# Optimization experiments

Hardware: AMD Instinct MI355X
Metric: run time of the kernel (lower is better)

## Reference

```python
import jax, jax.numpy as jnp
import numpy as np

IN_DIM = 256
HID = 384
HEADS = 6
NH1 = HID // HEADS  # 64 per-head hidden in layer1
N = 3072
SLOPE_GAT = 0.2   # LeakyReLU inside GAT attention
SLOPE_ACT = 0.01  # default nn.LeakyReLU / F.leaky_relu slope


def _leaky(x, s):
    return jnp.where(x >= 0, x, s * x)


def _gat_sublayer(h, mask, W, a, heads, nh, concat):
    # h: [N, F_in], mask: [N, N] bool, W: [heads*nh, F_in], a: [2*nh]
    n = h.shape[0]
    g = (h @ W.T).reshape(n, heads, nh)  # [N, H, F]
    # e[i,j,h] = leakyrelu(<g_i, a_l> + <g_j, a_r>)  (avoids O(N^2) concat)
    sl = jnp.einsum('nhf,f->nh', g, a[:nh])
    sr = jnp.einsum('nhf,f->nh', g, a[nh:])
    e = _leaky(sl[:, None, :] + sr[None, :, :], SLOPE_GAT)  # [N, N, H]
    e = jnp.where(mask[:, :, None], e, jnp.float32(-10000.0))
    att = jax.nn.softmax(e, axis=1)  # softmax over source nodes j
    out = jnp.einsum('ijh,jhf->ihf', att, g)
    return out.reshape(n, heads * nh) if concat else out.mean(axis=1)


def _gat(x, mask, W1, a1, W2, a2):
    x = _gat_sublayer(x, mask, W1, a1, HEADS, NH1, True)   # [N, HID]
    x = jax.nn.elu(x)
    return _gat_sublayer(x, mask, W2, a2, 1, IN_DIM, False)  # [N, IN_DIM]


def setup_inputs() -> dict:
    key = jax.random.key(0)
    ks = iter(jax.random.split(key, 32))
    d = {
        'feature': jax.random.normal(next(ks), (1, N, IN_DIM), jnp.float32),
        'adj': jax.random.randint(next(ks), (1, N, N), 0, 2, jnp.int32),
        'doc_num': 16,
        'sect_num': 192,
    }
    def w(shape, scale=0.05):
        return jax.random.normal(next(ks), shape, jnp.float32) * scale
    for br in ('sent', 'sect', 'doc'):
        d[f'W1_{br}'] = w((HID, IN_DIM))
        d[f'a1_{br}'] = w((2 * NH1,))
        d[f'W2_{br}'] = w((IN_DIM, HID))
        d[f'a2_{br}'] = w((2 * IN_DIM,))
    d['fusion_W'] = w((IN_DIM, 3 * IN_DIM)); d['fusion_b'] = jnp.zeros((IN_DIM,), jnp.float32)
    d['ffn_W0'] = w((HID, IN_DIM)); d['ffn_b0'] = jnp.zeros((HID,), jnp.float32)
    d['ffn_W1'] = w((HID, HID)); d['ffn_b1'] = jnp.zeros((HID,), jnp.float32)
    d['ffn_W2'] = w((IN_DIM, HID)); d['ffn_b2'] = jnp.zeros((IN_DIM,), jnp.float32)
    return d


def reference(feature, adj, doc_num, sect_num,
              W1_sent, a1_sent, W2_sent, a2_sent,
              W1_sect, a1_sect, W2_sect, a2_sect,
              W1_doc, a1_doc, W2_doc, a2_doc,
              fusion_W, fusion_b,
              ffn_W0, ffn_b0, ffn_W1, ffn_b1, ffn_W2, ffn_b2):
    f = feature[0]          # [N, D]
    n = f.shape[0]
    A = adj[0] != 0         # [N, N]
    cols = jnp.arange(n)
    sent_mask = A & (cols < n - sect_num - doc_num)[None, :]
    sect_mask = A & (cols >= n - sect_num - doc_num)[None, :] & (cols < n - doc_num)[None, :]
    doc_mask = A & (cols >= n - doc_num)[None, :]

    f_sent = _gat(f, sent_mask, W1_sent, a1_sent, W2_sent, a2_sent) + f
    f_sect = _gat(f, sect_mask, W1_sect, a1_sect, W2_sect, a2_sect) + f
    f_doc = _gat(f, doc_mask, W1_doc, a1_doc, W2_doc, a2_doc) + f

    fused = jnp.concatenate([f_doc, f_sect, f_sent], axis=-1)  # [N, 3D]
    fused = _leaky(fused @ fusion_W.T + fusion_b, SLOPE_ACT)
    h = _leaky(fused @ ffn_W0.T + ffn_b0, SLOPE_ACT)
    h = _leaky(h @ ffn_W1.T + ffn_b1, SLOPE_ACT)
    h = _leaky(h @ ffn_W2.T + ffn_b2, SLOPE_ACT)
    return (h + f)[None]    # [1, N, D]
```

## Files before the change

kernel.cpp:

```cpp
#include <hip/hip_runtime.h>
#include <stdint.h>

#define N_NODES 3072
#define D_IN    256
#define HIDDEN  384
#define HEADS   6
#define NH1     64
#define C1      1152
#define C2      768
#define MASK_ULL   48
#define MT_STRIDE  ((size_t)384 * N_NODES)
#define QS      6
#define LOG2E   1.4426950408889634f

typedef __bf16 bf16;
typedef __bf16 bf16x8 __attribute__((ext_vector_type(8)));
typedef __bf16 bf16x4 __attribute__((ext_vector_type(4)));
typedef float  f32x4  __attribute__((ext_vector_type(4)));

typedef __attribute__((address_space(1))) const unsigned int as1_u32;
typedef __attribute__((address_space(3))) unsigned int as3_u32;

__device__ __forceinline__ void gload_lds16(const void* g, void* l) {
  __builtin_amdgcn_global_load_lds((as1_u32*)g, (as3_u32*)l, 16, 0, 0);
}
__device__ __forceinline__ void gload_lds4(const void* g, void* l) {
  __builtin_amdgcn_global_load_lds((as1_u32*)g, (as3_u32*)l, 4, 0, 0);
}

__device__ __forceinline__ void atomAddF(float* p, float v) {
  __hip_atomic_fetch_add(p, v, __ATOMIC_RELAXED, __HIP_MEMORY_SCOPE_AGENT);
}
__device__ __forceinline__ float fexp2(float x) {
  float r; asm("v_exp_f32 %0, %1" : "=v"(r) : "v"(x)); return r;
}
__device__ __forceinline__ int bnd32(int jlo, int jhi, int len, int q, int Qb) {
  return (q >= Qb) ? ((jhi + 31) & ~31) : ((jlo + (len * q) / Qb) & ~31);
}

struct CastArgs {
  const float* src[11];
  bf16*        dst[11];
  int          cum4[12];
  int          castN;
};

__global__ __launch_bounds__(256) void prep_kernel(CastArgs A,
                                                   const int* __restrict__ adj,
                                                   unsigned char* __restrict__ maskT,
                                                   const int* __restrict__ dnum,
                                                   const int* __restrict__ snum) {
  if ((int)blockIdx.x < A.castN) {
    int g = blockIdx.x * 256 + threadIdx.x;
    int j = 0;
#pragma unroll
    for (int k = 1; k < 11; ++k) j += (g >= A.cum4[k]);
    int e = (g - A.cum4[j]) * 4;
    float4 v = *(const float4*)(A.src[j] + e);
    bf16x4 o = { (bf16)v.x, (bf16)v.y, (bf16)v.z, (bf16)v.w };
    *(bf16x4*)(A.dst[j] + e) = o;
    return;
  }
  int dn = dnum[0], sn = snum[0];
  int bb1 = N_NODES - sn - dn, bb2 = N_NODES - dn;
  int row = blockIdx.x - A.castN;
  const int* ar = adj + (size_t)row * N_NODES;
  int lane = threadIdx.x & 63, wave = threadIdx.x >> 6;
#pragma unroll
  for (int it = 0; it < N_NODES / 256; ++it) {
    int j = it * 256 + wave * 64 + lane;
    bool a = ar[j] != 0;
    unsigned long long m0 = __ballot(a && (j < bb1));
    unsigned long long m1 = __ballot(a && (j >= bb1) && (j < bb2));
    unsigned long long m2 = __ballot(a && (j >= bb2));
    int moBase = it * 32 + wave * 8;
    if (lane < 8)
      maskT[(size_t)(moBase + lane) * N_NODES + row] = (unsigned char)(m0 >> (lane * 8));
    else if (lane < 16)
      maskT[MT_STRIDE + (size_t)(moBase + lane - 8) * N_NODES + row] = (unsigned char)(m1 >> ((lane - 8) * 8));
    else if (lane < 24)
      maskT[2 * MT_STRIDE + (size_t)(moBase + lane - 16) * N_NODES + row] = (unsigned char)(m2 >> ((lane - 16) * 8));
  }
}

template<int C>
__global__ __launch_bounds__(256) void pack_kernel(const bf16* __restrict__ src,
                                                   bf16* __restrict__ dst,
                                                   float* __restrict__ gm) {
  __shared__ bf16 t[64][72];
  int j0 = blockIdx.x * 64, f0 = blockIdx.y * 64;
  int rr = threadIdx.x >> 4;
  int cc = (threadIdx.x & 15) * 4;
#pragma unroll
  for (int p = 0; p < 4; ++p) {
    int r = p * 16 + rr;
    *(bf16x4*)&t[r][cc] = *(const bf16x4*)&src[(size_t)(j0 + r) * C + f0 + cc];
  }
  __syncthreads();
  int f = threadIdx.x & 63, g = threadIdx.x >> 6;
#pragma unroll
  for (int q = 0; q < 2; ++q) {
    int p = g * 2 + q;
    bf16x8 v = { t[p*8+0][f], t[p*8+1][f], t[p*8+2][f], t[p*8+3][f],
                 t[p*8+4][f], t[p*8+5][f], t[p*8+6][f], t[p*8+7][f] };
    *(bf16x8*)&dst[ ((size_t)((j0 >> 3) + p) * C + f0 + f) * 8 ] = v;
  }
  float s = 0.f;
#pragma unroll
  for (int k = 0; k < 16; ++k) s += (float)t[g * 16 + k][f];
  atomAddF(&gm[f0 + f], s * (1.0f / N_NODES));
}

template<int NCPB, int NH>
__global__ __launch_bounds__(256) void head_proj_kernel(
    const bf16* __restrict__ g, int ldg,
    const float* __restrict__ a0, const float* __restrict__ a1, const float* __restrict__ a2,
    float* __restrict__ elp, float* __restrict__ eln,
    float* __restrict__ erp, float* __restrict__ ern) {
  int c = blockIdx.y;
  int i = blockIdx.x * 16 + (threadIdx.x >> 4);
  int b = c / NCPB;
  const float* a = (b == 0) ? a0 : (b == 1) ? a1 : a2;
  int f0 = (threadIdx.x & 15) * (NH / 16);
  const bf16* gr = g + (size_t)i * ldg + c * NH + f0;
  float accl = 0.f, accr = 0.f;
#pragma unroll
  for (int k = 0; k < NH / 16; k += 4) {
    bf16x4 v = *(const bf16x4*)&gr[k];
#pragma unroll
    for (int e = 0; e < 4; ++e) {
      float gv = (float)v[e];
      accl += gv * a[f0 + k + e];
      accr += gv * a[NH + f0 + k + e];
    }
  }
#pragma unroll
  for (int m = 1; m < 16; m <<= 1) {
    accl += __shfl_xor(accl, m, 64);
    accr += __shfl_xor(accr, m, 64);
  }
  if ((threadIdx.x & 15) == 0) {
    int o = c * N_NODES + i;
    elp[o] = fexp2(accl * LOG2E);
    eln[o] = fexp2(0.2f * accl * LOG2E);
    erp[o] = fexp2(accr * LOG2E);
    ern[o] = fexp2(0.2f * accr * LOG2E);
  }
}

template<bool BIAS, bool LEAKY, bool RES, bool F32OUT>
__global__ __launch_bounds__(256) void gemm64_kernel(
    const bf16* __restrict__ A, int lda, int aZoff,
    const bf16* __restrict__ B0, const bf16* __restrict__ B1, const bf16* __restrict__ B2,
    int ldb, void* __restrict__ Cout, int ldc, int cZoff, int K,
    const float* __restrict__ bias, const float* __restrict__ res) {
  __shared__ bf16 As[2 * 64 * 64];
  __shared__ bf16 Bs[2 * 64 * 64];
  int z = blockIdx.z;
  const bf16* Ab = A + (size_t)z * aZoff;
  const bf16* Bb = (z == 0) ? B0 : (z == 1) ? B1 : B2;
  int m0 = blockIdx.x * 64, n0 = blockIdx.y * 64;
  int tid = threadIdx.x;
  int lane = tid & 63, wave = tid >> 6;
  int wm = wave >> 1, wn = wave & 1;
  int l15 = lane & 15, lk = lane >> 4;
  int r0 = tid >> 3, p0 = tid & 7, q0 = p0 ^ (r0 & 7);
  int r1 = (256 + tid) >> 3, p1 = tid & 7, q1 = p1 ^ (r1 & 7);
  bf16x8 ra0, ra1, rb0, rb1;
  auto gload = [&](int kt) {
    const bf16* ab = Ab + (size_t)kt * 64;
    const bf16* bb = Bb + (size_t)kt * 64;
    ra0 = *(const bf16x8*)&ab[(size_t)(m0 + r0) * lda + q0 * 8];
    ra1 = *(const bf16x8*)&ab[(size_t)(m0 + r1) * lda + q1 * 8];
    rb0 = *(const bf16x8*)&bb[(size_t)(n0 + r0) * ldb + q0 * 8];
    rb1 = *(const bf16x8*)&bb[(size_t)(n0 + r1) * ldb + q1 * 8];
  };
  auto sstore = [&](int buf) {
    bf16* as = As + buf * 4096;
    bf16* bs = Bs + buf * 4096;
    *(bf16x8*)&as[r0 * 64 + p0 * 8] = ra0;
    *(bf16x8*)&as[r1 * 64 + p1 * 8] = ra1;
    *(bf16x8*)&bs[r0 * 64 + p0 * 8] = rb0;
    *(bf16x8*)&bs[r1 * 64 + p1 * 8] = rb1;
  };
  f32x4 acc[2][2] = {};
  int nk = K >> 6;
  gload(0);
  sstore(0);
  __syncthreads();
  for (int kt = 0; kt < nk; ++kt) {
    bool more = (kt + 1) < nk;
    if (more) gload(kt + 1);
    const bf16* as = As + (kt & 1) * 4096;
    const bf16* bs = Bs + (kt & 1) * 4096;
#pragma unroll
    for (int s = 0; s < 2; ++s) {
      bf16x8 af[2], bfr[2];
      int u = s * 4 + lk;
#pragma unroll
      for (int mi = 0; mi < 2; ++mi) {
        int r = wm * 32 + mi * 16 + l15;
        af[mi] = *(const bf16x8*)&as[r * 64 + (u ^ (r & 7)) * 8];
      }
#pragma unroll
      for (int ni = 0; ni < 2; ++ni) {
        int r = wn * 32 + ni * 16 + l15;
        bfr[ni] = *(const bf16x8*)&bs[r * 64 + (u ^ (r & 7)) * 8];
      }
#pragma unroll
      for (int mi = 0; mi < 2; ++mi)
#pragma unroll
        for (int ni = 0; ni < 2; ++ni)
          acc[mi][ni] = __builtin_amdgcn_mfma_f32_16x16x32_bf16(af[mi], bfr[ni], acc[mi][ni], 0, 0, 0);
    }
    if (more) sstore((kt + 1) & 1);
    __syncthreads();
  }
#pragma unroll
  for (int mi = 0; mi < 2; ++mi)
#pragma unroll
    for (int ni = 0; ni < 2; ++ni)
#pragma unroll
      for (int r = 0; r < 4; ++r) {
        int i = m0 + wm * 32 + mi * 16 + lk * 4 + r;
        int col = z * cZoff + n0 + wn * 32 + ni * 16 + l15;
        float v = acc[mi][ni][r];
        if (BIAS) v += bias[col];
        if (LEAKY) v = (v >= 0.f) ? v : 0.01f * v;
        if (RES) v += res[(size_t)i * ldc + col];
        if (F32OUT) ((float*)Cout)[(size_t)i * ldc + col] = v;
        else        ((bf16*)Cout)[(size_t)i * ldc + col] = (bf16)v;
      }
}

template<bool L1>
__global__ __launch_bounds__(256, 2) void att_kernel(
    const bf16* __restrict__ gP,
    const float* __restrict__ elpA, const float* __restrict__ elnA,
    const float* __restrict__ erpA, const float* __restrict__ ernA,
    const unsigned char* __restrict__ maskT,
    const int* __restrict__ dnum, const int* __restrict__ snum,
    float* __restrict__ accP, float* __restrict__ lP) {
  constexpr int C = L1 ? C1 : C2;
  int c = blockIdx.y;
  int b = L1 ? (c / 6) : (c >> 2);
  int colbase = L1 ? c * 64 : (b * 256 + (c & 3) * 64);
  int sidx = L1 ? c : b;
  int q = blockIdx.z;
  int Qb = (b == 0) ? QS : 1;
  if (q >= Qb) return;
  int dn = dnum[0], sn = snum[0];
  int bb1 = N_NODES - sn - dn, bb2 = N_NODES - dn;
  int jlo = (b == 0) ? 0 : (b == 1) ? bb1 : bb2;
  int jhi = (b == 0) ? bb1 : (b == 1) ? bb2 : N_NODES;
  int len = jhi - jlo;
  int wlo = bnd32(jlo, jhi, len, q, Qb);
  int whi = bnd32(jlo, jhi, len, q + 1, Qb);
  if (wlo >= whi) return;

  __shared__ bf16  sgP[2][8][64 * 8];
  __shared__ float serp[2][64];
  __shared__ float sern[2][64];

  int wave = threadIdx.x >> 6, lane = threadIdx.x & 63;
  int l15 = lane & 15, lk = lane >> 4;
  int row0 = blockIdx.x * 256 + wave * 64;
  float elp[4], eln[4];
#pragma unroll
  for (int rg = 0; rg < 4; ++rg) {
    int ip = row0 + rg * 16 + l15;
    elp[rg] = elpA[sidx * N_NODES + ip];
    eln[rg] = elnA[sidx * N_NODES + ip];
  }
  const float* erpB = erpA + sidx * N_NODES;
  const float* ernB = ernA + sidx * N_NODES;
  const bf16* gPcol = gP + (size_t)colbase * 8;
  const unsigned char* mTb = maskT + (size_t)b * MT_STRIDE;
  bf16x8 ones;
#pragma unroll
  for (int e = 0; e < 8; ++e) ones[e] = (bf16)1.0f;
  f32x4 acc[4][4] = {};
  f32x4 accl[4] = {};

  auto stage = [&](int buf, int cb) {
    int mo0 = cb >> 3;
#pragma unroll
    for (int k = 0; k < 2; ++k) {
      int ml = wave * 2 + k;
      if ((mo0 + ml) * 8 < whi)
        gload_lds16(gPcol + ((size_t)(mo0 + ml) * C + lane) * 8, &sgP[buf][ml][0]);
    }
    if (wave == 0) gload_lds4(erpB + cb + lane, &serp[buf][0]);
    if (wave == 1) gload_lds4(ernB + cb + lane, &sern[buf][0]);
  };

  int buf = 0;
  stage(0, wlo);
  asm volatile("s_waitcnt vmcnt(0)" ::: "memory");
  __syncthreads();
  for (int cb = wlo; cb < whi; cb += 64) {
    int nb = cb + 64;
    if (nb < whi) stage(buf ^ 1, nb);
#pragma unroll
    for (int h = 0; h < 2; ++h) {
      int jt = cb + h * 32;
      if (jt >= whi) break;
      int lj = h * 32 + lk * 8;
      int oct = h * 4 + lk;
      f32x4 pv0 = *(const f32x4*)&serp[buf][lj];
      f32x4 pv1 = *(const f32x4*)&serp[buf][lj + 4];
      f32x4 nv0 = *(const f32x4*)&sern[buf][lj];
      f32x4 nv1 = *(const f32x4*)&sern[buf][lj + 4];
      bf16x8 bf0 = *(const bf16x8*)&sgP[buf][oct][(0 * 16 + l15) * 8];
      bf16x8 bf1 = *(const bf16x8*)&sgP[buf][oct][(1 * 16 + l15) * 8];
      bf16x8 bf2 = *(const bf16x8*)&sgP[buf][oct][(2 * 16 + l15) * 8];
      bf16x8 bf3 = *(const bf16x8*)&sgP[buf][oct][(3 * 16 + l15) * 8];
      const unsigned char* mT = mTb + (size_t)((jt >> 3) + lk) * N_NODES + row0;
#pragma unroll
      for (int rg = 0; rg < 4; ++rg) {
        unsigned int mb = mT[rg * 16 + l15];
        bf16x8 a8;
#pragma unroll
        for (int e = 0; e < 8; ++e) {
          float pvv = (e < 4) ? pv0[e & 3] : pv1[e & 3];
          float nvv = (e < 4) ? nv0[e & 3] : nv1[e & 3];
          float z = elp[rg] * pvv;
          float w = eln[rg] * nvv;
          float p = (z >= 1.f) ? z : w;
          p = ((mb >> e) & 1u) ? p : 0.f;
          a8[e] = (bf16)p;
        }
        acc[rg][0] = __builtin_amdgcn_mfma_f32_16x16x32_bf16(a8, bf0, acc[rg][0], 0, 0, 0);
        acc[rg][1] = __builtin_amdgcn_mfma_f32_16x16x32_bf16(a8, bf1, acc[rg][1], 0, 0, 0);
        acc[rg][2] = __builtin_amdgcn_mfma_f32_16x16x32_bf16(a8, bf2, acc[rg][2], 0, 0, 0);
        acc[rg][3] = __builtin_amdgcn_mfma_f32_16x16x32_bf16(a8, bf3, acc[rg][3], 0, 0, 0);
        accl[rg]   = __builtin_amdgcn_mfma_f32_16x16x32_bf16(a8, ones, accl[rg], 0, 0, 0);
      }
    }
    asm volatile("s_waitcnt vmcnt(0)" ::: "memory");
    __syncthreads();
    buf ^= 1;
  }

  int slot = (b == 0) ? (c * QS + q) : (L1 ? (36 + (c - 6)) : (24 + (c - 4)));
  float* ap = accP + ((size_t)slot * N_NODES + row0) * 64;
#pragma unroll
  for (int rg = 0; rg < 4; ++rg)
#pragma unroll
    for (int nf = 0; nf < 4; ++nf)
#pragma unroll
      for (int r = 0; r < 4; ++r)
        ap[(rg * 16 + lk * 4 + r) * 64 + nf * 16 + l15] = acc[rg][nf][r];
  if (l15 == 0) {
#pragma unroll
    for (int rg = 0; rg < 4; ++rg)
#pragma unroll
      for (int r = 0; r < 4; ++r)
        lP[(size_t)slot * N_NODES + row0 + rg * 16 + lk * 4 + r] = accl[rg][r];
  }
}

__global__ __launch_bounds__(256) void fin1_kernel(
    const float* __restrict__ accP, const float* __restrict__ lP,
    const float* __restrict__ gm, const int* __restrict__ dnum, const int* __restrict__ snum,
    bf16* __restrict__ out1) {
  int t = blockIdx.x * 256 + threadIdx.x;
  int i = t / (C1 / 8), f0 = (t - i * (C1 / 8)) * 8;
  int c = f0 >> 6;
  int b = c / 6;
  int dn = dnum[0], sn = snum[0];
  int bb1 = N_NODES - sn - dn, bb2 = N_NODES - dn;
  int jlo = (b == 0) ? 0 : (b == 1) ? bb1 : bb2;
  int jhi = (b == 0) ? bb1 : (b == 1) ? bb2 : N_NODES;
  int len = jhi - jlo;
  int Qb = (b == 0) ? QS : 1;
  float l = 0.f;
  float a[8] = {0.f,0.f,0.f,0.f,0.f,0.f,0.f,0.f};
  if (len > 0) {
    for (int q = 0; q < Qb; ++q) {
      if (bnd32(jlo, jhi, len, q, Qb) >= bnd32(jlo, jhi, len, q + 1, Qb)) continue;
      int slot = (b == 0) ? (c * QS + q) : (36 + (c - 6));
      l += lP[(size_t)slot * N_NODES + i];
      const float* ap = &accP[((size_t)slot * N_NODES + i) * 64 + (f0 & 63)];
      f32x4 v0 = *(const f32x4*)ap, v1 = *(const f32x4*)(ap + 4);
#pragma unroll
      for (int e = 0; e < 4; ++e) { a[e] += v0[e]; a[e + 4] += v1[e]; }
    }
  }
  float inv = (l > 0.f) ? 1.f / l : 0.f;
  bf16x8 o;
#pragma unroll
  for (int e = 0; e < 8; ++e) {
    float v = (l > 0.f) ? a[e] * inv : gm[f0 + e];
    v = (v > 0.f) ? v : (__expf(v) - 1.f);
    o[e] = (bf16)v;
  }
  *(bf16x8*)&out1[(size_t)i * C1 + f0] = o;
}

__global__ __launch_bounds__(256) void fin2_kernel(
    const float* __restrict__ accP, const float* __restrict__ lP,
    const float* __restrict__ gm, const float* __restrict__ feat,
    const int* __restrict__ dnum, const int* __restrict__ snum,
    bf16* __restrict__ fused) {
  int t = blockIdx.x * 256 + threadIdx.x;
  int i = t / (C2 / 8), f0 = (t - i * (C2 / 8)) * 8;
  int b = f0 >> 8;
  int fi = f0 & 255;
  int fc = (f0 >> 6) & 3;
  int c = b * 4 + fc;
  int dn = dnum[0], sn = snum[0];
  int bb1 = N_NODES - sn - dn, bb2 = N_NODES - dn;
  int jlo = (b == 0) ? 0 : (b == 1) ? bb1 : bb2;
  int jhi = (b == 0) ? bb1 : (b == 1) ? bb2 : N_NODES;
  int len = jhi - jlo;
  int Qb = (b == 0) ? QS : 1;
  float l = 0.f;
  float a[8] = {0.f,0.f,0.f,0.f,0.f,0.f,0.f,0.f};
  if (len > 0) {
    for (int q = 0; q < Qb; ++q) {
      if (bnd32(jlo, jhi, len, q, Qb) >= bnd32(jlo, jhi, len, q + 1, Qb)) continue;
      int slot = (b == 0) ? (c * QS + q) : (24 + (c - 4));
      l += lP[(size_t)slot * N_NODES + i];
      const float* ap = &accP[((size_t)slot * N_NODES + i) * 64 + (f0 & 63)];
      f32x4 v0 = *(const f32x4*)ap, v1 = *(const f32x4*)(ap + 4);
#pragma unroll
      for (int e = 0; e < 4; ++e) { a[e] += v0[e]; a[e + 4] += v1[e]; }
    }
  }
  float inv = (l > 0.f) ? 1.f / l : 0.f;
  bf16x8 o;
#pragma unroll
  for (int e = 0; e < 8; ++e) {
    float v = (l > 0.f) ? a[e] * inv : gm[f0 + e];
    v += feat[(size_t)i * D_IN + fi + e];
    o[e] = (bf16)v;
  }
  *(bf16x8*)&fused[(size_t)i * C2 + (2 - b) * D_IN + fi] = o;
}

extern "C" void kernel_launch(void* const* d_in, const int* in_sizes, int n_in,
                              void* d_out, int out_size, void* d_ws, size_t ws_size,
                              hipStream_t stream) {
  (void)in_sizes; (void)n_in; (void)out_size; (void)ws_size;
  const float* feature = (const float*)d_in[0];
  const int*   adj     = (const int*)d_in[1];
  const int*   dnum    = (const int*)d_in[2];
  const int*   snum    = (const int*)d_in[3];
  const float* W1s = (const float*)d_in[4];  const float* a1s = (const float*)d_in[5];
  const float* W2s = (const float*)d_in[6];  const float* a2s = (const float*)d_in[7];
  const float* W1e = (const float*)d_in[8];  const float* a1e = (const float*)d_in[9];
  const float* W2e = (const float*)d_in[10]; const float* a2e = (const float*)d_in[11];
  const float* W1d = (const float*)d_in[12]; const float* a1d = (const float*)d_in[13];
  const float* W2d = (const float*)d_in[14]; const float* a2d = (const float*)d_in[15];
  const float* fW  = (const float*)d_in[16]; const float* fB  = (const float*)d_in[17];
  const float* w0  = (const float*)d_in[18]; const float* b0  = (const float*)d_in[19];
  const float* w1  = (const float*)d_in[20]; const float* b1  = (const float*)d_in[21];
  const float* w2  = (const float*)d_in[22]; const float* b2  = (const float*)d_in[23];

  char* ws = (char*)d_ws;
  size_t off = 0;
  auto alloc = [&](size_t bytes) { void* p = ws + off; off += (bytes + 255) & ~(size_t)255; return p; };

  unsigned char* maskT = (unsigned char*)alloc(3 * MT_STRIDE);
  bf16* fbf   = (bf16*)alloc((size_t)N_NODES * D_IN * 2);
  bf16* w1b0  = (bf16*)alloc(HIDDEN * D_IN * 2);
  bf16* w1b1  = (bf16*)alloc(HIDDEN * D_IN * 2);
  bf16* w1b2  = (bf16*)alloc(HIDDEN * D_IN * 2);
  bf16* w2b0  = (bf16*)alloc(D_IN * HIDDEN * 2);
  bf16* w2b1  = (bf16*)alloc(D_IN * HIDDEN * 2);
  bf16* w2b2  = (bf16*)alloc(D_IN * HIDDEN * 2);
  bf16* wfusb = (bf16*)alloc(D_IN * C2 * 2);
  bf16* wf0b  = (bf16*)alloc(HIDDEN * D_IN * 2);
  bf16* wf1b  = (bf16*)alloc(HIDDEN * HIDDEN * 2);
  bf16* wf2b  = (bf16*)alloc(D_IN * HIDDEN * 2);
  bf16* g1    = (bf16*)alloc((size_t)N_NODES * C1 * 2);
  bf16* gP1   = (bf16*)alloc((size_t)N_NODES * C1 * 2);
  bf16* out1  = (bf16*)alloc((size_t)N_NODES * C1 * 2);
  bf16* g2    = (bf16*)alloc((size_t)N_NODES * C2 * 2);
  bf16* gP2   = (bf16*)alloc((size_t)N_NODES * C2 * 2);
  bf16* fusedB= (bf16*)alloc((size_t)N_NODES * C2 * 2);
  bf16* h0    = (bf16*)alloc((size_t)N_NODES * D_IN * 2);
  bf16* h1    = (bf16*)alloc((size_t)N_NODES * HIDDEN * 2);
  bf16* h2    = (bf16*)alloc((size_t)N_NODES * HIDDEN * 2);
  float* elp1 = (float*)alloc(18 * N_NODES * 4);
  float* eln1 = (float*)alloc(18 * N_NODES * 4);
  float* erp1 = (float*)alloc(18 * N_NODES * 4);
  float* ern1 = (float*)alloc(18 * N_NODES * 4);
  float* elp2 = (float*)alloc(3 * N_NODES * 4);
  float* eln2 = (float*)alloc(3 * N_NODES * 4);
  float* erp2 = (float*)alloc(3 * N_NODES * 4);
  float* ern2 = (float*)alloc(3 * N_NODES * 4);
  float* accU = (float*)alloc((size_t)48 * N_NODES * 64 * 4);
  float* lU   = (float*)alloc((size_t)48 * N_NODES * 4);
  size_t zoff = off;
  float* gm1  = (float*)alloc(C1 * 4);
  float* gm2  = (float*)alloc(C2 * 4);
  size_t zbytes = off - zoff;

  hipMemsetAsync(ws + zoff, 0, zbytes, stream);

  CastArgs ca;
  {
    const float* srcs[11] = { feature, W1s, W1e, W1d, W2s, W2e, W2d, fW, w0, w1, w2 };
    bf16* dsts[11] = { fbf, w1b0, w1b1, w1b2, w2b0, w2b1, w2b2, wfusb, wf0b, wf1b, wf2b };
    int counts[11] = { N_NODES*D_IN, HIDDEN*D_IN, HIDDEN*D_IN, HIDDEN*D_IN,
                       D_IN*HIDDEN, D_IN*HIDDEN, D_IN*HIDDEN, D_IN*C2,
                       HIDDEN*D_IN, HIDDEN*HIDDEN, D_IN*HIDDEN };
    int cum = 0;
    for (int k = 0; k < 11; ++k) { ca.src[k] = srcs[k]; ca.dst[k] = dsts[k]; ca.cum4[k] = cum; cum += counts[k] / 4; }
    ca.cum4[11] = cum;
    ca.castN = cum / 256;
    prep_kernel<<<ca.castN + N_NODES, 256, 0, stream>>>(ca, adj, maskT, dnum, snum);
  }
  gemm64_kernel<false,false,false,false><<<dim3(48,6,3), 256, 0, stream>>>(
      fbf, D_IN, 0, w1b0, w1b1, w1b2, D_IN, g1, C1, HIDDEN, D_IN, nullptr, nullptr);
  pack_kernel<C1><<<dim3(48,18), 256, 0, stream>>>(g1, gP1, gm1);
  head_proj_kernel<HEADS, NH1><<<dim3(192,18), 256, 0, stream>>>(g1, C1, a1s, a1e, a1d, elp1, eln1, erp1, ern1);
  att_kernel<true><<<dim3(12, 18, QS), 256, 0, stream>>>(gP1, elp1, eln1, erp1, ern1, maskT, dnum, snum, accU, lU);
  fin1_kernel<<<N_NODES * (C1 / 8) / 256, 256, 0, stream>>>(accU, lU, gm1, dnum, snum, out1);
  gemm64_kernel<false,false,false,false><<<dim3(48,4,3), 256, 0, stream>>>(
      out1, C1, HIDDEN, w2b0, w2b1, w2b2, HIDDEN, g2, C2, D_IN, HIDDEN, nullptr, nullptr);
  pack_kernel<C2><<<dim3(48,12), 256, 0, stream>>>(g2, gP2, gm2);
  head_proj_kernel<1, D_IN><<<dim3(192,3), 256, 0, stream>>>(g2, C2, a2s, a2e, a2d, elp2, eln2, erp2, ern2);
  att_kernel<false><<<dim3(12, 12, QS), 256, 0, stream>>>(gP2, elp2, eln2, erp2, ern2, maskT, dnum, snum, accU, lU);
  fin2_kernel<<<N_NODES * (C2 / 8) / 256, 256, 0, stream>>>(accU, lU, gm2, feature, dnum, snum, fusedB);
  gemm64_kernel<true,true,false,false><<<dim3(48,4,1), 256, 0, stream>>>(
      fusedB, C2, 0, wfusb, wfusb, wfusb, C2, h0, D_IN, 0, C2, fB, nullptr);
  gemm64_kernel<true,true,false,false><<<dim3(48,6,1), 256, 0, stream>>>(
      h0, D_IN, 0, wf0b, wf0b, wf0b, D_IN, h1, HIDDEN, 0, D_IN, b0, nullptr);
  gemm64_kernel<true,true,false,false><<<dim3(48,6,1), 256, 0, stream>>>(
      h1, HIDDEN, 0, wf1b, wf1b, wf1b, HIDDEN, h2, HIDDEN, 0, HIDDEN, b1, nullptr);
  gemm64_kernel<true,true,true,true><<<dim3(48,4,1), 256, 0, stream>>>(
      h2, HIDDEN, 0, wf2b, wf2b, wf2b, HIDDEN, d_out, D_IN, 0, HIDDEN, b2, feature);
}
```

Measured before the change: 291.7 us.

## Store single transposed adjacency bitmask and fold layer-1 head projection into pack

Replaces the three per-branch transposed masks with one shared transposed adjacency bitmask, built through an LDS tile so global writes are coalesced 32-bit stores instead of scattered bytes. The attention kernel now derives the branch column-range mask on the fly with a per-octet bit range. The layer-1 head projection (attention logits and their exponentials) is computed inside the pack kernel from the already-staged tile, removing one launch and a reread of g1. This cuts mask bandwidth and kernel count but adds a little ALU work per mask load in the attention loop.

```diff
diff --git a/kernel.cpp b/kernel.cpp
--- a/kernel.cpp
+++ b/kernel.cpp
@@ -8,8 +8,6 @@
 #define NH1     64
 #define C1      1152
 #define C2      768
-#define MASK_ULL   48
-#define MT_STRIDE  ((size_t)384 * N_NODES)
 #define QS      6
 #define LOG2E   1.4426950408889634f
 
@@ -47,9 +45,7 @@
 
 __global__ __launch_bounds__(256) void prep_kernel(CastArgs A,
                                                    const int* __restrict__ adj,
-                                                   unsigned char* __restrict__ maskT,
-                                                   const int* __restrict__ dnum,
-                                                   const int* __restrict__ snum) {
+                                                   unsigned char* __restrict__ adjT) {
   if ((int)blockIdx.x < A.castN) {
     int g = blockIdx.x * 256 + threadIdx.x;
     int j = 0;
@@ -61,32 +57,43 @@
     *(bf16x4*)(A.dst[j] + e) = o;
     return;
   }
-  int dn = dnum[0], sn = snum[0];
-  int bb1 = N_NODES - sn - dn, bb2 = N_NODES - dn;
-  int row = blockIdx.x - A.castN;
-  const int* ar = adj + (size_t)row * N_NODES;
-  int lane = threadIdx.x & 63, wave = threadIdx.x >> 6;
-#pragma unroll
-  for (int it = 0; it < N_NODES / 256; ++it) {
-    int j = it * 256 + wave * 64 + lane;
-    bool a = ar[j] != 0;
-    unsigned long long m0 = __ballot(a && (j < bb1));
-    unsigned long long m1 = __ballot(a && (j >= bb1) && (j < bb2));
-    unsigned long long m2 = __ballot(a && (j >= bb2));
-    int moBase = it * 32 + wave * 8;
-    if (lane < 8)
-      maskT[(size_t)(moBase + lane) * N_NODES + row] = (unsigned char)(m0 >> (lane * 8));
-    else if (lane < 16)
-      maskT[MT_STRIDE + (size_t)(moBase + lane - 8) * N_NODES + row] = (unsigned char)(m1 >> ((lane - 8) * 8));
-    else if (lane < 24)
-      maskT[2 * MT_STRIDE + (size_t)(moBase + lane - 16) * N_NODES + row] = (unsigned char)(m2 >> ((lane - 16) * 8));
-  }
-}
-
-template<int C>
+  int blk = blockIdx.x - A.castN;
+  int rb = blk >> 3, jb = blk & 7;
+  int row0 = rb * 64, jbase = jb * 384;
+  __shared__ unsigned char tile[48][64];
+  int wave = threadIdx.x >> 6, lane = threadIdx.x & 63;
+#pragma unroll
+  for (int rr = 0; rr < 16; ++rr) {
+    int row = wave * 16 + rr;
+    const int* ar = adj + (size_t)(row0 + row) * N_NODES + jbase;
+#pragma unroll
+    for (int it = 0; it < 6; ++it) {
+      unsigned long long m = __ballot(ar[it * 64 + lane] != 0);
+      if (lane < 8) tile[it * 8 + lane][row] = (unsigned char)(m >> (lane * 8));
+    }
+  }
+  __syncthreads();
+  const unsigned int* tu = (const unsigned int*)&tile[0][0];
+  unsigned int* gu = (unsigned int*)adjT;
+#pragma unroll
+  for (int k = 0; k < 3; ++k) {
+    int idx = k * 256 + threadIdx.x;
+    int mo = idx >> 4, rw = idx & 15;
+    gu[((size_t)((jbase >> 3) + mo)) * (N_NODES / 4) + (row0 >> 2) + rw] = tu[mo * 16 + rw];
+  }
+}
+
+template<int C, bool FOLD>
 __global__ __launch_bounds__(256) void pack_kernel(const bf16* __restrict__ src,
                                                    bf16* __restrict__ dst,
-                                                   float* __restrict__ gm) {
+                                                   float* __restrict__ gm,
+                                                   const float* __restrict__ pa0,
+                                                   const float* __restrict__ pa1,
+                                                   const float* __restrict__ pa2,
+                                                   float* __restrict__ elp,
+                                                   float* __restrict__ eln,
+                                                   float* __restrict__ erp,
+                                                   float* __restrict__ ern) {
   __shared__ bf16 t[64][72];
   int j0 = blockIdx.x * 64, f0 = blockIdx.y * 64;
   int rr = threadIdx.x >> 4;
@@ -109,6 +116,29 @@
 #pragma unroll
   for (int k = 0; k < 16; ++k) s += (float)t[g * 16 + k][f];
   atomAddF(&gm[f0 + f], s * (1.0f / N_NODES));
+  if constexpr (FOLD) {
+    int cmb = f0 >> 6;
+    int b = cmb / 6;
+    const float* a = (b == 0) ? pa0 : (b == 1) ? pa1 : pa2;
+    int r = threadIdx.x >> 2;
+    int part = (threadIdx.x & 3) * 16;
+    float dl = 0.f, dr = 0.f;
+#pragma unroll
+    for (int k = 0; k < 16; ++k) {
+      float gv = (float)t[r][part + k];
+      dl += gv * a[part + k];
+      dr += gv * a[64 + part + k];
+    }
+    dl += __shfl_xor(dl, 1, 64); dr += __shfl_xor(dr, 1, 64);
+    dl += __shfl_xor(dl, 2, 64); dr += __shfl_xor(dr, 2, 64);
+    if ((threadIdx.x & 3) == 0) {
+      int o = cmb * N_NODES + j0 + r;
+      elp[o] = fexp2(dl * LOG2E);
+      eln[o] = fexp2(0.2f * dl * LOG2E);
+      erp[o] = fexp2(dr * LOG2E);
+      ern[o] = fexp2(0.2f * dr * LOG2E);
+    }
+  }
 }
 
 template<int NCPB, int NH>
@@ -238,7 +268,7 @@
     const bf16* __restrict__ gP,
     const float* __restrict__ elpA, const float* __restrict__ elnA,
     const float* __restrict__ erpA, const float* __restrict__ ernA,
-    const unsigned char* __restrict__ maskT,
+    const unsigned char* __restrict__ adjT,
     const int* __restrict__ dnum, const int* __restrict__ snum,
     float* __restrict__ accP, float* __restrict__ lP) {
   constexpr int C = L1 ? C1 : C2;
@@ -275,7 +305,6 @@
   const float* erpB = erpA + sidx * N_NODES;
   const float* ernB = ernA + sidx * N_NODES;
   const bf16* gPcol = gP + (size_t)colbase * 8;
-  const unsigned char* mTb = maskT + (size_t)b * MT_STRIDE;
   bf16x8 ones;
 #pragma unroll
   for (int e = 0; e < 8; ++e) ones[e] = (bf16)1.0f;
@@ -307,6 +336,11 @@
       if (jt >= whi) break;
       int lj = h * 32 + lk * 8;
       int oct = h * 4 + lk;
+      int mo = (jt >> 3) + lk;
+      int j0o = mo << 3;
+      int lo = min(max(jlo - j0o, 0), 8);
+      int hi = min(max(jhi - j0o, 0), 8);
+      unsigned int rb_ = ((1u << hi) - 1u) & ~((1u << lo) - 1u);
       f32x4 pv0 = *(const f32x4*)&serp[buf][lj];
       f32x4 pv1 = *(const f32x4*)&serp[buf][lj + 4];
       f32x4 nv0 = *(const f32x4*)&sern[buf][lj];
@@ -315,10 +349,10 @@
       bf16x8 bf1 = *(const bf16x8*)&sgP[buf][oct][(1 * 16 + l15) * 8];
       bf16x8 bf2 = *(const bf16x8*)&sgP[buf][oct][(2 * 16 + l15) * 8];
       bf16x8 bf3 = *(const bf16x8*)&sgP[buf][oct][(3 * 16 + l15) * 8];
-      const unsigned char* mT = mTb + (size_t)((jt >> 3) + lk) * N_NODES + row0;
+      const unsigned char* mT = adjT + (size_t)mo * N_NODES + row0;
 #pragma unroll
       for (int rg = 0; rg < 4; ++rg) {
-        unsigned int mb = mT[rg * 16 + l15];
+        unsigned int mb = mT[rg * 16 + l15] & rb_;
         bf16x8 a8;
 #pragma unroll
         for (int e = 0; e < 8; ++e) {
@@ -462,7 +496,7 @@
   size_t off = 0;
   auto alloc = [&](size_t bytes) { void* p = ws + off; off += (bytes + 255) & ~(size_t)255; return p; };
 
-  unsigned char* maskT = (unsigned char*)alloc(3 * MT_STRIDE);
+  unsigned char* adjT = (unsigned char*)alloc((size_t)384 * N_NODES);
   bf16* fbf   = (bf16*)alloc((size_t)N_NODES * D_IN * 2);
   bf16* w1b0  = (bf16*)alloc(HIDDEN * D_IN * 2);
   bf16* w1b1  = (bf16*)alloc(HIDDEN * D_IN * 2);
@@ -511,19 +545,19 @@
     for (int k = 0; k < 11; ++k) { ca.src[k] = srcs[k]; ca.dst[k] = dsts[k]; ca.cum4[k] = cum; cum += counts[k] / 4; }
     ca.cum4[11] = cum;
     ca.castN = cum / 256;
-    prep_kernel<<<ca.castN + N_NODES, 256, 0, stream>>>(ca, adj, maskT, dnum, snum);
+    prep_kernel<<<ca.castN + 384, 256, 0, stream>>>(ca, adj, adjT);
   }
   gemm64_kernel<false,false,false,false><<<dim3(48,6,3), 256, 0, stream>>>(
       fbf, D_IN, 0, w1b0, w1b1, w1b2, D_IN, g1, C1, HIDDEN, D_IN, nullptr, nullptr);
-  pack_kernel<C1><<<dim3(48,18), 256, 0, stream>>>(g1, gP1, gm1);
-  head_proj_kernel<HEADS, NH1><<<dim3(192,18), 256, 0, stream>>>(g1, C1, a1s, a1e, a1d, elp1, eln1, erp1, ern1);
-  att_kernel<true><<<dim3(12, 18, QS), 256, 0, stream>>>(gP1, elp1, eln1, erp1, ern1, maskT, dnum, snum, accU, lU);
+  pack_kernel<C1,true><<<dim3(48,18), 256, 0, stream>>>(g1, gP1, gm1, a1s, a1e, a1d, elp1, eln1, erp1, ern1);
+  att_kernel<true><<<dim3(12, 18, QS), 256, 0, stream>>>(gP1, elp1, eln1, erp1, ern1, adjT, dnum, snum, accU, lU);
   fin1_kernel<<<N_NODES * (C1 / 8) / 256, 256, 0, stream>>>(accU, lU, gm1, dnum, snum, out1);
   gemm64_kernel<false,false,false,false><<<dim3(48,4,3), 256, 0, stream>>>(
       out1, C1, HIDDEN, w2b0, w2b1, w2b2, HIDDEN, g2, C2, D_IN, HIDDEN, nullptr, nullptr);
-  pack_kernel<C2><<<dim3(48,12), 256, 0, stream>>>(g2, gP2, gm2);
+  pack_kernel<C2,false><<<dim3(48,12), 256, 0, stream>>>(g2, gP2, gm2,
+      nullptr, nullptr, nullptr, nullptr, nullptr, nullptr, nullptr);
   head_proj_kernel<1, D_IN><<<dim3(192,3), 256, 0, stream>>>(g2, C2, a2s, a2e, a2d, elp2, eln2, erp2, ern2);
-  att_kernel<false><<<dim3(12, 12, QS), 256, 0, stream>>>(gP2, elp2, eln2, erp2, ern2, maskT, dnum, snum, accU, lU);
+  att_kernel<false><<<dim3(12, 12, QS), 256, 0, stream>>>(gP2, elp2, eln2, erp2, ern2, adjT, dnum, snum, accU, lU);
   fin2_kernel<<<N_NODES * (C2 / 8) / 256, 256, 0, stream>>>(accU, lU, gm2, feature, dnum, snum, fusedB);
   gemm64_kernel<true,true,false,false><<<dim3(48,4,1), 256, 0, stream>>>(
       fusedB, C2, 0, wfusb, wfusb, wfusb, C2, h0, D_IN, 0, C2, fB, nullptr);
```

Result: slower. 307.9 us (+5.6%).
